# Optimization experiments

Hardware: AMD Instinct MI355X
Metric: run time of the kernel (lower is better)

## Reference

```python
import jax, jax.numpy as jnp
import numpy as np


def _soft_proto(x, P):
    d2 = (x * x).sum(-1, keepdims=True) - 2.0 * (x @ P.T) + (P * P).sum(-1)
    w = jax.nn.softmax(-d2, axis=-1)  # scores = -dist_sq, softmax over K
    return w @ P  # soft-matched prototypes


def setup_inputs() -> dict:
    key = jax.random.key(0)
    ks = jax.random.split(key, 12)
    B = 1024
    def u(k, shape, s=0.1):
        return jax.random.uniform(k, shape, minval=-s, maxval=s, dtype=jnp.float32)
    return {
        "fcn": jax.random.normal(ks[0], (B, 90, 90), jnp.float32),
        "scn": jax.random.normal(ks[1], (B, 90, 90), jnp.float32),
        # node embedding Linear(90->48), weights stored [in,out]
        "W_node": u(ks[2], (90, 48)), "b_node": jnp.zeros((48,), jnp.float32),
        "P_node": u(ks[3], (64, 48)),   # node prototypes, init uniform(-0.1,0.1)
        "W_graph": u(ks[4], (48, 32)), "b_graph": jnp.zeros((32,), jnp.float32),
        "P_graph": u(ks[5], (32, 32)),
        "Wg1": u(ks[6], (32, 32)), "bg1": jnp.zeros((32,), jnp.float32),
        "Wg2": u(ks[7], (32, 16)), "bg2": jnp.zeros((16,), jnp.float32),
        "P_cls": u(ks[8], (16, 16)),
        # classifier: final_dim = 2*90*48 + 2*32 + 2*16 = 8736
        "Wc1": u(ks[9], (8736, 256)), "bc1": jnp.zeros((256,), jnp.float32),
        "Wc2": u(ks[10], (256, 3)), "bc2": jnp.zeros((3,), jnp.float32),
    }


def reference(fcn, scn, W_node, b_node, P_node, W_graph, b_graph, P_graph,
              Wg1, bg1, Wg2, bg2, P_cls, Wc1, bc1, Wc2, bc2):
    def branch(x):
        nodes = x @ W_node + b_node                  # [B,90,48]
        nm = _soft_proto(nodes, P_node)              # [B,90,48]
        eg = nm.mean(axis=1) @ W_graph + b_graph     # [B,32]
        gp = _soft_proto(eg, P_graph)                # [B,32]
        ec = jax.nn.relu(gp @ Wg1 + bg1) @ Wg2 + bg2 # [B,16]
        cp = _soft_proto(ec, P_cls)                  # [B,16]
        return nm, gp, cp

    nmf, gpf, cpf = branch(fcn)
    nms, gps, cps = branch(scn)
    B = fcn.shape[0]
    R = jnp.concatenate(
        [nmf.reshape(B, -1), nms.reshape(B, -1), gpf, gps, cpf, cps], axis=-1)  # [B,8736]
    # dropout(0.5) is identity in eval mode
    logits = jax.nn.relu(R @ Wc1 + bc1) @ Wc2 + bc2  # [B,3]
    return logits
```

## Files before the change

kernel.cpp:

```cpp
#include <hip/hip_runtime.h>
#include <hip/hip_bf16.h>

using f16   = _Float16;
using f16x4 = __attribute__((ext_vector_type(4))) _Float16;
using f16x8 = __attribute__((ext_vector_type(8))) _Float16;
using f32x4 = __attribute__((ext_vector_type(4))) float;

__global__ __launch_bounds__(256) void prep_kernel(
    const float* __restrict__ Wn, const float* __restrict__ Pn,
    f16* __restrict__ wf, float* __restrict__ q)
{
  int i = blockIdx.x * 256 + threadIdx.x;
  if (i < 4992) {
    int n = i / 104, k = i - n * 104;
    wf[i] = (k < 90) ? (f16)Wn[k * 48 + n] : (f16)0.f;
  } else if (i < 8576) {
    int j = i - 4992; int p = j / 56, c = j - p * 56;
    wf[i] = (c < 48) ? (f16)Pn[p * 48 + c] : (f16)0.f;
  } else if (i < 12032) {
    int j = i - 8576; int r = j / 72, p = j - r * 72;
    wf[i] = (p < 64) ? (f16)Pn[p * 48 + r] : (f16)0.f;
  } else if (i < 12096) {
    int p = i - 12032;
    float s = 0.f;
    for (int j = 0; j < 48; ++j) { float v = Pn[p * 48 + j]; s = fmaf(v, v, s); }
    q[p] = s;
  }
}

__global__ __launch_bounds__(256) void wc1t_kernel(
    const float* __restrict__ Wc1, f16* __restrict__ Wc1T)
{
  __shared__ f16 sT[32 * 36];
  const int tid = threadIdx.x;
  const int kt = blockIdx.x, ct = blockIdx.y;
  const int c = tid & 31, r4 = (tid >> 5) * 4;
  #pragma unroll
  for (int i = 0; i < 4; ++i) {
    int r = r4 + i;
    sT[c * 36 + r] = (f16)Wc1[(size_t)(kt * 32 + r) * 256 + ct * 32 + c];
  }
  __syncthreads();
  #pragma unroll
  for (int i = 0; i < 4; ++i) {
    int r = r4 + i;
    Wc1T[(size_t)(ct * 32 + r) * 8736 + kt * 32 + c] = sT[r * 36 + c];
  }
}

__global__ __launch_bounds__(256, 6) void node_kernel(
    const float* __restrict__ fcn, const float* __restrict__ scn,
    const float* __restrict__ bn, const f16* __restrict__ wf,
    const float* __restrict__ qg,
    f16* __restrict__ R, float* __restrict__ nmmean)
{
  __shared__ __align__(16) f16 sW[96 * 72];
  __shared__ __align__(16) f16 sNodes[96 * 56];
  __shared__ float sQ[64];
  __shared__ float sCol[4][3][16];

  const f16* Pw   = wf + 4992;
  const f16* PnTw = wf + 8576;

  const int tid = threadIdx.x;
  const int lane = tid & 63, wv = tid >> 6;
  const int l15 = lane & 15, lg = lane >> 4;
  const int b = blockIdx.x, br = blockIdx.y;
  const float* x = (br ? scn : fcn) + (size_t)b * 8100;

  if (tid < 64) sQ[tid] = qg[tid];

  for (int mt = wv; mt < 6; mt += 4) {
    const int row = mt * 16 + l15;
    const float* xrow = x + row * 90;
    f16x8 a[3];
    #pragma unroll
    for (int kt = 0; kt < 3; ++kt) {
      const int k0 = kt * 32 + lg * 8;
      f16x8 h;
      #pragma unroll
      for (int e = 0; e < 8; ++e) h[e] = (f16)0.f;
      if (row < 90) {
        const float* src = xrow + k0;
        if (k0 < 88) {
          float2 u0 = *(const float2*)(src + 0);
          float2 u1 = *(const float2*)(src + 2);
          float2 u2 = *(const float2*)(src + 4);
          float2 u3 = *(const float2*)(src + 6);
          h[0] = (f16)u0.x; h[1] = (f16)u0.y; h[2] = (f16)u1.x; h[3] = (f16)u1.y;
          h[4] = (f16)u2.x; h[5] = (f16)u2.y; h[6] = (f16)u3.x; h[7] = (f16)u3.y;
        } else {
          float2 u0 = *(const float2*)src;
          h[0] = (f16)u0.x; h[1] = (f16)u0.y;
        }
      }
      a[kt] = h;
    }
    #pragma unroll
    for (int nt = 0; nt < 3; ++nt) {
      f32x4 acc = {0.f, 0.f, 0.f, 0.f};
      #pragma unroll
      for (int kt = 0; kt < 3; ++kt) {
        f16x8 bb = *(const f16x8*)&wf[(nt * 16 + l15) * 104 + kt * 32 + lg * 8];
        acc = __builtin_amdgcn_mfma_f32_16x16x32_f16(a[kt], bb, acc, 0, 0, 0);
      }
      const float bias = bn[nt * 16 + l15];
      #pragma unroll
      for (int r = 0; r < 4; ++r)
        sNodes[(mt * 16 + lg * 4 + r) * 56 + nt * 16 + l15] = (f16)(acc[r] + bias);
    }
  }
  __syncthreads();

  for (int mt = wv; mt < 6; mt += 4) {
    f32x4 acc[4];
    #pragma unroll
    for (int nt = 0; nt < 4; ++nt) acc[nt] = (f32x4){0.f, 0.f, 0.f, 0.f};
    const f16x8 a0 = *(const f16x8*)&sNodes[(mt * 16 + l15) * 56 + lg * 8];
    const f16x4 a1 = *(const f16x4*)&sNodes[(mt * 16 + l15) * 56 + 32 + lg * 4];
    #pragma unroll
    for (int nt = 0; nt < 4; ++nt) {
      f16x8 b0 = *(const f16x8*)&Pw[(nt * 16 + l15) * 56 + lg * 8];
      acc[nt] = __builtin_amdgcn_mfma_f32_16x16x32_f16(a0, b0, acc[nt], 0, 0, 0);
      f16x4 b1 = *(const f16x4*)&Pw[(nt * 16 + l15) * 56 + 32 + lg * 4];
      acc[nt] = __builtin_amdgcn_mfma_f32_16x16x16f16(a1, b1, acc[nt], 0, 0, 0);
    }
    float qv[4];
    #pragma unroll
    for (int nt = 0; nt < 4; ++nt) qv[nt] = sQ[nt * 16 + l15];
    #pragma unroll
    for (int r = 0; r < 4; ++r) {
      float s0 = 2.f * acc[0][r] - qv[0];
      float s1 = 2.f * acc[1][r] - qv[1];
      float s2 = 2.f * acc[2][r] - qv[2];
      float s3 = 2.f * acc[3][r] - qv[3];
      float m = fmaxf(fmaxf(s0, s1), fmaxf(s2, s3));
      m = fmaxf(m, __shfl_xor(m, 1, 64));
      m = fmaxf(m, __shfl_xor(m, 2, 64));
      m = fmaxf(m, __shfl_xor(m, 4, 64));
      m = fmaxf(m, __shfl_xor(m, 8, 64));
      float e0 = __expf(s0 - m), e1 = __expf(s1 - m);
      float e2 = __expf(s2 - m), e3 = __expf(s3 - m);
      float sum = (e0 + e1) + (e2 + e3);
      sum += __shfl_xor(sum, 1, 64);
      sum += __shfl_xor(sum, 2, 64);
      sum += __shfl_xor(sum, 4, 64);
      sum += __shfl_xor(sum, 8, 64);
      const float inv = 1.f / sum;
      const int row = mt * 16 + lg * 4 + r;
      sW[row * 72 + 0 * 16 + l15] = (f16)(e0 * inv);
      sW[row * 72 + 1 * 16 + l15] = (f16)(e1 * inv);
      sW[row * 72 + 2 * 16 + l15] = (f16)(e2 * inv);
      sW[row * 72 + 3 * 16 + l15] = (f16)(e3 * inv);
    }
  }
  __syncthreads();

  f16* Rrow = R + (size_t)b * 8736 + (size_t)br * 4320;
  float cs[3] = {0.f, 0.f, 0.f};
  for (int t = wv; t < 18; t += 4) {
    const int mt = t / 3, nt = t - 3 * mt;
    f32x4 acc = {0.f, 0.f, 0.f, 0.f};
    #pragma unroll
    for (int kt = 0; kt < 2; ++kt) {
      f16x8 a  = *(const f16x8*)&sW[(mt * 16 + l15) * 72 + kt * 32 + lg * 8];
      f16x8 bb = *(const f16x8*)&PnTw[(nt * 16 + l15) * 72 + kt * 32 + lg * 8];
      acc = __builtin_amdgcn_mfma_f32_16x16x32_f16(a, bb, acc, 0, 0, 0);
    }
    #pragma unroll
    for (int r = 0; r < 4; ++r) {
      const int row = mt * 16 + lg * 4 + r;
      if (row < 90) {
        Rrow[row * 48 + nt * 16 + l15] = (f16)acc[r];
        cs[nt] += acc[r];
      }
    }
  }
  #pragma unroll
  for (int nt = 0; nt < 3; ++nt) {
    cs[nt] += __shfl_xor(cs[nt], 16, 64);
    cs[nt] += __shfl_xor(cs[nt], 32, 64);
  }
  if (lane < 16) {
    sCol[wv][0][lane] = cs[0];
    sCol[wv][1][lane] = cs[1];
    sCol[wv][2][lane] = cs[2];
  }
  __syncthreads();
  if (tid < 48) {
    const int nt = tid >> 4, c = tid & 15;
    float s = sCol[0][nt][c] + sCol[1][nt][c] + sCol[2][nt][c] + sCol[3][nt][c];
    nmmean[((size_t)br * 1024 + b) * 48 + tid] = s * (1.f / 90.f);
  }
}

__global__ __launch_bounds__(256) void graph_kernel(
    const float* __restrict__ nmmean,
    const float* __restrict__ Wg, const float* __restrict__ bg,
    const float* __restrict__ Pg,
    const float* __restrict__ Wg1, const float* __restrict__ bg1,
    const float* __restrict__ Wg2, const float* __restrict__ bg2,
    const float* __restrict__ Pc,
    f16* __restrict__ R)
{
  __shared__ float sE[4][64];
  __shared__ float sT[4][64];
  const int tid = threadIdx.x;
  const int wid = tid >> 6, lane = tid & 63;
  const int idx = blockIdx.x * 4 + wid;
  const int br = idx >> 10, b = idx & 1023;
  const float* mrow = nmmean + (size_t)idx * 48;
  f16* Rrow = R + (size_t)b * 8736;

  if (lane < 32) {
    float e = bg[lane];
    #pragma unroll
    for (int k = 0; k < 48; ++k) e = fmaf(mrow[k], Wg[k * 32 + lane], e);
    sE[wid][lane] = e;
  }
  __syncthreads();
  if (lane < 32) {
    float s = 0.f;
    #pragma unroll
    for (int j = 0; j < 32; ++j) { float pv = Pg[lane * 32 + j]; s += pv * (2.f * sE[wid][j] - pv); }
    float m = s;
    for (int d = 16; d >= 1; d >>= 1) m = fmaxf(m, __shfl_xor(m, d, 64));
    float ex = __expf(s - m);
    float sum = ex;
    for (int d = 16; d >= 1; d >>= 1) sum += __shfl_xor(sum, d, 64);
    sT[wid][lane] = ex / sum;
  }
  __syncthreads();
  if (lane < 32) {
    float g = 0.f;
    #pragma unroll
    for (int p = 0; p < 32; ++p) g = fmaf(sT[wid][p], Pg[p * 32 + lane], g);
    Rrow[8640 + br * 32 + lane] = (f16)g;
    sE[wid][lane] = g;
  }
  __syncthreads();
  if (lane < 32) {
    float h = bg1[lane];
    #pragma unroll
    for (int k = 0; k < 32; ++k) h = fmaf(sE[wid][k], Wg1[k * 32 + lane], h);
    sT[wid][lane] = fmaxf(h, 0.f);
  }
  __syncthreads();
  if (lane < 16) {
    float c = bg2[lane];
    #pragma unroll
    for (int k = 0; k < 32; ++k) c = fmaf(sT[wid][k], Wg2[k * 16 + lane], c);
    sE[wid][lane] = c;
  }
  __syncthreads();
  if (lane < 16) {
    float s = 0.f;
    #pragma unroll
    for (int j = 0; j < 16; ++j) { float pv = Pc[lane * 16 + j]; s += pv * (2.f * sE[wid][j] - pv); }
    float m = s;
    for (int d = 8; d >= 1; d >>= 1) m = fmaxf(m, __shfl_xor(m, d, 64));
    float ex = __expf(s - m);
    float sum = ex;
    for (int d = 8; d >= 1; d >>= 1) sum += __shfl_xor(sum, d, 64);
    sT[wid][lane] = ex / sum;
  }
  __syncthreads();
  if (lane < 16) {
    float c = 0.f;
    #pragma unroll
    for (int p = 0; p < 16; ++p) c = fmaf(sT[wid][p], Pc[p * 16 + lane], c);
    Rrow[8704 + br * 16 + lane] = (f16)c;
  }
}

__global__ __launch_bounds__(256) void gemm1_kernel(
    const f16* __restrict__ R, const f16* __restrict__ Wc1T,
    float* __restrict__ part, int KS)
{
  __shared__ __align__(16) f16 sA[128 * 40];
  __shared__ __align__(16) f16 sB[64 * 40];
  const int tid = threadIdx.x;
  const int lane = tid & 63, wv = tid >> 6;
  const int l15 = lane & 15, lg = lane >> 4;
  const int wm = wv >> 1, wn = wv & 1;
  const int bm = blockIdx.x * 128, bnc = blockIdx.y * 64, z = blockIdx.z;
  const int base = 273 / KS, rem = 273 - base * KS;
  const int t0 = z * base + (z < rem ? z : rem);
  const int nt_ = base + (z < rem ? 1 : 0);
  const int kbeg = t0 * 32, kend = (t0 + nt_) * 32;

  const int ar = tid >> 1, ah = (tid & 1) * 16;
  const int bc = tid >> 2, bh = (tid & 3) * 8;

  f32x4 acc[4][2];
  #pragma unroll
  for (int mt = 0; mt < 4; ++mt)
    #pragma unroll
    for (int nt = 0; nt < 2; ++nt) acc[mt][nt] = (f32x4){0.f, 0.f, 0.f, 0.f};

  f16x8 v0 = *(const f16x8*)&R[(size_t)(bm + ar) * 8736 + kbeg + ah];
  f16x8 v1 = *(const f16x8*)&R[(size_t)(bm + ar) * 8736 + kbeg + ah + 8];
  f16x8 w0 = *(const f16x8*)&Wc1T[(size_t)(bnc + bc) * 8736 + kbeg + bh];

  for (int kk = kbeg; kk < kend; kk += 32) {
    *(f16x8*)&sA[ar * 40 + ah] = v0;
    *(f16x8*)&sA[ar * 40 + ah + 8] = v1;
    *(f16x8*)&sB[bc * 40 + bh] = w0;
    __syncthreads();
    if (kk + 32 < kend) {
      v0 = *(const f16x8*)&R[(size_t)(bm + ar) * 8736 + kk + 32 + ah];
      v1 = *(const f16x8*)&R[(size_t)(bm + ar) * 8736 + kk + 32 + ah + 8];
      w0 = *(const f16x8*)&Wc1T[(size_t)(bnc + bc) * 8736 + kk + 32 + bh];
    }
    #pragma unroll
    for (int mt = 0; mt < 4; ++mt) {
      f16x8 a = *(const f16x8*)&sA[(wm * 64 + mt * 16 + l15) * 40 + lg * 8];
      #pragma unroll
      for (int nt = 0; nt < 2; ++nt) {
        f16x8 bb = *(const f16x8*)&sB[(wn * 32 + nt * 16 + l15) * 40 + lg * 8];
        acc[mt][nt] = __builtin_amdgcn_mfma_f32_16x16x32_f16(a, bb, acc[mt][nt], 0, 0, 0);
      }
    }
    __syncthreads();
  }
  float* pz = part + (size_t)z * 262144;
  #pragma unroll
  for (int mt = 0; mt < 4; ++mt)
    #pragma unroll
    for (int nt = 0; nt < 2; ++nt)
      #pragma unroll
      for (int r = 0; r < 4; ++r)
        pz[(size_t)(bm + wm * 64 + mt * 16 + lg * 4 + r) * 256 +
           bnc + wn * 32 + nt * 16 + l15] = acc[mt][nt][r];
}

__global__ __launch_bounds__(256) void head_kernel(
    const float* __restrict__ part, const float* __restrict__ bc1,
    const float* __restrict__ Wc2, const float* __restrict__ bc2,
    float* __restrict__ out, int KS)
{
  __shared__ float red[3][4];
  const int b = blockIdx.x, t = threadIdx.x;
  float s0 = 0.f, s1 = 0.f, s2 = 0.f, s3 = 0.f;
  int z = 0;
  for (; z + 4 <= KS; z += 4) {
    s0 += part[(size_t)(z + 0) * 262144 + (size_t)b * 256 + t];
    s1 += part[(size_t)(z + 1) * 262144 + (size_t)b * 256 + t];
    s2 += part[(size_t)(z + 2) * 262144 + (size_t)b * 256 + t];
    s3 += part[(size_t)(z + 3) * 262144 + (size_t)b * 256 + t];
  }
  for (; z < KS; ++z) s0 += part[(size_t)z * 262144 + (size_t)b * 256 + t];
  float acc = bc1[t] + ((s0 + s1) + (s2 + s3));
  float h = fmaxf(acc, 0.f);
  float p0 = h * Wc2[t * 3 + 0];
  float p1 = h * Wc2[t * 3 + 1];
  float p2 = h * Wc2[t * 3 + 2];
  for (int d = 32; d >= 1; d >>= 1) {
    p0 += __shfl_xor(p0, d, 64);
    p1 += __shfl_xor(p1, d, 64);
    p2 += __shfl_xor(p2, d, 64);
  }
  const int wid = t >> 6, lane = t & 63;
  if (lane == 0) { red[0][wid] = p0; red[1][wid] = p1; red[2][wid] = p2; }
  __syncthreads();
  if (t < 3) {
    out[(size_t)b * 3 + t] = red[t][0] + red[t][1] + red[t][2] + red[t][3] + bc2[t];
  }
}

extern "C" void kernel_launch(void* const* d_in, const int* in_sizes, int n_in,
                              void* d_out, int out_size, void* d_ws, size_t ws_size,
                              hipStream_t stream) {
  const float* fcn     = (const float*)d_in[0];
  const float* scn     = (const float*)d_in[1];
  const float* W_node  = (const float*)d_in[2];
  const float* b_node  = (const float*)d_in[3];
  const float* P_node  = (const float*)d_in[4];
  const float* W_graph = (const float*)d_in[5];
  const float* b_graph = (const float*)d_in[6];
  const float* P_graph = (const float*)d_in[7];
  const float* Wg1     = (const float*)d_in[8];
  const float* bg1     = (const float*)d_in[9];
  const float* Wg2     = (const float*)d_in[10];
  const float* bg2     = (const float*)d_in[11];
  const float* P_cls   = (const float*)d_in[12];
  const float* Wc1     = (const float*)d_in[13];
  const float* bc1     = (const float*)d_in[14];
  const float* Wc2     = (const float*)d_in[15];
  const float* bc2     = (const float*)d_in[16];
  float* out = (float*)d_out;

  char* ws = (char*)d_ws;
  f16*   R16    = (f16*)ws;
  f16*   Wc1T   = (f16*)(ws + 17891328);
  f16*   wf     = (f16*)(ws + 22364160);
  float* qbuf   = (float*)(ws + 22388224);
  float* nmmean = (float*)(ws + 22388480);
  float* part   = (float*)(ws + 22781696);

  size_t avail = ws_size > 22781696u ? ws_size - 22781696u : 0;
  int KS = (int)(avail / 1048576u);
  if (KS > 16) KS = 16;
  if (KS < 1) KS = 1;

  prep_kernel<<<48, 256, 0, stream>>>(W_node, P_node, wf, qbuf);
  wc1t_kernel<<<dim3(273, 8), 256, 0, stream>>>(Wc1, Wc1T);
  node_kernel<<<dim3(1024, 2), 256, 0, stream>>>(fcn, scn, b_node, wf, qbuf,
                                                 R16, nmmean);
  graph_kernel<<<512, 256, 0, stream>>>(nmmean, W_graph, b_graph, P_graph,
                                        Wg1, bg1, Wg2, bg2, P_cls, R16);
  gemm1_kernel<<<dim3(8, 4, KS), 256, 0, stream>>>(R16, Wc1T, part, KS);
  head_kernel<<<1024, 256, 0, stream>>>(part, bc1, Wc2, bc2, out, KS);
}
```

Baseline: 70.15 us.

## Give each wave one 16-row tile in node kernel and drop block barriers

The node kernel now launches 384 threads so each of six waves owns one 16-row tile through all three stages: node embedding, prototype softmax and soft-match output. Intermediates sit in a per-wave shared scratch and are guarded only by lgkmcnt waits, which removes two block-wide __syncthreads and the imbalance of 4 waves covering 6 tiles. It also cuts shared memory per block and reads q straight from global. The risk is lower occupancy from the larger block size and the removed launch_bounds min-blocks hint, which may raise register use.

```diff
diff --git a/kernel.cpp b/kernel.cpp
--- a/kernel.cpp
+++ b/kernel.cpp
@@ -48,16 +48,15 @@
   }
 }
 
-__global__ __launch_bounds__(256, 6) void node_kernel(
+__global__ __launch_bounds__(384) void node_kernel(
     const float* __restrict__ fcn, const float* __restrict__ scn,
     const float* __restrict__ bn, const f16* __restrict__ wf,
     const float* __restrict__ qg,
     f16* __restrict__ R, float* __restrict__ nmmean)
 {
-  __shared__ __align__(16) f16 sW[96 * 72];
-  __shared__ __align__(16) f16 sNodes[96 * 56];
+  __shared__ __align__(16) f16 sS[6][1152];
   __shared__ float sQ[64];
-  __shared__ float sCol[4][3][16];
+  __shared__ float sCol[6][3][16];
 
   const f16* Pw   = wf + 4992;
   const f16* PnTw = wf + 8576;
@@ -67,111 +66,110 @@
   const int l15 = lane & 15, lg = lane >> 4;
   const int b = blockIdx.x, br = blockIdx.y;
   const float* x = (br ? scn : fcn) + (size_t)b * 8100;
+  f16* scr = sS[wv];
 
   if (tid < 64) sQ[tid] = qg[tid];
 
-  for (int mt = wv; mt < 6; mt += 4) {
-    const int row = mt * 16 + l15;
-    const float* xrow = x + row * 90;
-    f16x8 a[3];
+  const int row = wv * 16 + l15;
+  const float* xrow = x + row * 90;
+  f16x8 a[3];
+  #pragma unroll
+  for (int kt = 0; kt < 3; ++kt) {
+    const int k0 = kt * 32 + lg * 8;
+    f16x8 h;
+    #pragma unroll
+    for (int e = 0; e < 8; ++e) h[e] = (f16)0.f;
+    if (row < 90) {
+      const float* src = xrow + k0;
+      if (k0 < 88) {
+        float2 u0 = *(const float2*)(src + 0);
+        float2 u1 = *(const float2*)(src + 2);
+        float2 u2 = *(const float2*)(src + 4);
+        float2 u3 = *(const float2*)(src + 6);
+        h[0] = (f16)u0.x; h[1] = (f16)u0.y; h[2] = (f16)u1.x; h[3] = (f16)u1.y;
+        h[4] = (f16)u2.x; h[5] = (f16)u2.y; h[6] = (f16)u3.x; h[7] = (f16)u3.y;
+      } else {
+        float2 u0 = *(const float2*)src;
+        h[0] = (f16)u0.x; h[1] = (f16)u0.y;
+      }
+    }
+    a[kt] = h;
+  }
+  #pragma unroll
+  for (int nt = 0; nt < 3; ++nt) {
+    f32x4 acc = {0.f, 0.f, 0.f, 0.f};
     #pragma unroll
     for (int kt = 0; kt < 3; ++kt) {
-      const int k0 = kt * 32 + lg * 8;
-      f16x8 h;
-      #pragma unroll
-      for (int e = 0; e < 8; ++e) h[e] = (f16)0.f;
-      if (row < 90) {
-        const float* src = xrow + k0;
-        if (k0 < 88) {
-          float2 u0 = *(const float2*)(src + 0);
-          float2 u1 = *(const float2*)(src + 2);
-          float2 u2 = *(const float2*)(src + 4);
-          float2 u3 = *(const float2*)(src + 6);
-          h[0] = (f16)u0.x; h[1] = (f16)u0.y; h[2] = (f16)u1.x; h[3] = (f16)u1.y;
-          h[4] = (f16)u2.x; h[5] = (f16)u2.y; h[6] = (f16)u3.x; h[7] = (f16)u3.y;
-        } else {
-          float2 u0 = *(const float2*)src;
-          h[0] = (f16)u0.x; h[1] = (f16)u0.y;
-        }
-      }
-      a[kt] = h;
+      f16x8 bb = *(const f16x8*)&wf[(nt * 16 + l15) * 104 + kt * 32 + lg * 8];
+      acc = __builtin_amdgcn_mfma_f32_16x16x32_f16(a[kt], bb, acc, 0, 0, 0);
     }
-    #pragma unroll
-    for (int nt = 0; nt < 3; ++nt) {
-      f32x4 acc = {0.f, 0.f, 0.f, 0.f};
-      #pragma unroll
-      for (int kt = 0; kt < 3; ++kt) {
-        f16x8 bb = *(const f16x8*)&wf[(nt * 16 + l15) * 104 + kt * 32 + lg * 8];
-        acc = __builtin_amdgcn_mfma_f32_16x16x32_f16(a[kt], bb, acc, 0, 0, 0);
-      }
-      const float bias = bn[nt * 16 + l15];
-      #pragma unroll
-      for (int r = 0; r < 4; ++r)
-        sNodes[(mt * 16 + lg * 4 + r) * 56 + nt * 16 + l15] = (f16)(acc[r] + bias);
-    }
-  }
-  __syncthreads();
-
-  for (int mt = wv; mt < 6; mt += 4) {
-    f32x4 acc[4];
-    #pragma unroll
-    for (int nt = 0; nt < 4; ++nt) acc[nt] = (f32x4){0.f, 0.f, 0.f, 0.f};
-    const f16x8 a0 = *(const f16x8*)&sNodes[(mt * 16 + l15) * 56 + lg * 8];
-    const f16x4 a1 = *(const f16x4*)&sNodes[(mt * 16 + l15) * 56 + 32 + lg * 4];
-    #pragma unroll
-    for (int nt = 0; nt < 4; ++nt) {
-      f16x8 b0 = *(const f16x8*)&Pw[(nt * 16 + l15) * 56 + lg * 8];
-      acc[nt] = __builtin_amdgcn_mfma_f32_16x16x32_f16(a0, b0, acc[nt], 0, 0, 0);
-      f16x4 b1 = *(const f16x4*)&Pw[(nt * 16 + l15) * 56 + 32 + lg * 4];
-      acc[nt] = __builtin_amdgcn_mfma_f32_16x16x16f16(a1, b1, acc[nt], 0, 0, 0);
-    }
-    float qv[4];
-    #pragma unroll
-    for (int nt = 0; nt < 4; ++nt) qv[nt] = sQ[nt * 16 + l15];
+    const float bias = bn[nt * 16 + l15];
+    #pragma unroll
+    for (int r = 0; r < 4; ++r)
+      scr[(lg * 4 + r) * 56 + nt * 16 + l15] = (f16)(acc[r] + bias);
+  }
+  asm volatile("s_waitcnt lgkmcnt(0)" ::: "memory");
+  __builtin_amdgcn_sched_barrier(0);
+
+  const f16x8 a0 = *(const f16x8*)&scr[l15 * 56 + lg * 8];
+  const f16x4 a1 = *(const f16x4*)&scr[l15 * 56 + 32 + lg * 4];
+  f32x4 acc2[4];
+  #pragma unroll
+  for (int nt = 0; nt < 4; ++nt) acc2[nt] = (f32x4){0.f, 0.f, 0.f, 0.f};
+  #pragma unroll
+  for (int nt = 0; nt < 4; ++nt) {
+    f16x8 b0 = *(const f16x8*)&Pw[(nt * 16 + l15) * 56 + lg * 8];
+    acc2[nt] = __builtin_amdgcn_mfma_f32_16x16x32_f16(a0, b0, acc2[nt], 0, 0, 0);
+    f16x4 b1 = *(const f16x4*)&Pw[(nt * 16 + l15) * 56 + 32 + lg * 4];
+    acc2[nt] = __builtin_amdgcn_mfma_f32_16x16x16f16(a1, b1, acc2[nt], 0, 0, 0);
+  }
+  float qv[4];
+  #pragma unroll
+  for (int nt = 0; nt < 4; ++nt) qv[nt] = qg[nt * 16 + l15];
+  #pragma unroll
+  for (int r = 0; r < 4; ++r) {
+    float s0 = 2.f * acc2[0][r] - qv[0];
+    float s1 = 2.f * acc2[1][r] - qv[1];
+    float s2 = 2.f * acc2[2][r] - qv[2];
+    float s3 = 2.f * acc2[3][r] - qv[3];
+    float m = fmaxf(fmaxf(s0, s1), fmaxf(s2, s3));
+    m = fmaxf(m, __shfl_xor(m, 1, 64));
+    m = fmaxf(m, __shfl_xor(m, 2, 64));
+    m = fmaxf(m, __shfl_xor(m, 4, 64));
+    m = fmaxf(m, __shfl_xor(m, 8, 64));
+    float e0 = __expf(s0 - m), e1 = __expf(s1 - m);
+    float e2 = __expf(s2 - m), e3 = __expf(s3 - m);
+    float sum = (e0 + e1) + (e2 + e3);
+    sum += __shfl_xor(sum, 1, 64);
+    sum += __shfl_xor(sum, 2, 64);
+    sum += __shfl_xor(sum, 4, 64);
+    sum += __shfl_xor(sum, 8, 64);
+    const float inv = 1.f / sum;
+    const int lr = lg * 4 + r;
+    scr[lr * 72 + 0 * 16 + l15] = (f16)(e0 * inv);
+    scr[lr * 72 + 1 * 16 + l15] = (f16)(e1 * inv);
+    scr[lr * 72 + 2 * 16 + l15] = (f16)(e2 * inv);
+    scr[lr * 72 + 3 * 16 + l15] = (f16)(e3 * inv);
+  }
+  asm volatile("s_waitcnt lgkmcnt(0)" ::: "memory");
+  __builtin_amdgcn_sched_barrier(0);
+
+  f16* Rrow = R + (size_t)b * 8736 + (size_t)br * 4320;
+  const f16x8 wa0 = *(const f16x8*)&scr[l15 * 72 + lg * 8];
+  const f16x8 wa1 = *(const f16x8*)&scr[l15 * 72 + 32 + lg * 8];
+  float cs[3] = {0.f, 0.f, 0.f};
+  #pragma unroll
+  for (int nt = 0; nt < 3; ++nt) {
+    f32x4 acc = {0.f, 0.f, 0.f, 0.f};
+    f16x8 b0 = *(const f16x8*)&PnTw[(nt * 16 + l15) * 72 + lg * 8];
+    acc = __builtin_amdgcn_mfma_f32_16x16x32_f16(wa0, b0, acc, 0, 0, 0);
+    f16x8 b1 = *(const f16x8*)&PnTw[(nt * 16 + l15) * 72 + 32 + lg * 8];
+    acc = __builtin_amdgcn_mfma_f32_16x16x32_f16(wa1, b1, acc, 0, 0, 0);
     #pragma unroll
     for (int r = 0; r < 4; ++r) {
-      float s0 = 2.f * acc[0][r] - qv[0];
-      float s1 = 2.f * acc[1][r] - qv[1];
-      float s2 = 2.f * acc[2][r] - qv[2];
-      float s3 = 2.f * acc[3][r] - qv[3];
-      float m = fmaxf(fmaxf(s0, s1), fmaxf(s2, s3));
-      m = fmaxf(m, __shfl_xor(m, 1, 64));
-      m = fmaxf(m, __shfl_xor(m, 2, 64));
-      m = fmaxf(m, __shfl_xor(m, 4, 64));
-      m = fmaxf(m, __shfl_xor(m, 8, 64));
-      float e0 = __expf(s0 - m), e1 = __expf(s1 - m);
-      float e2 = __expf(s2 - m), e3 = __expf(s3 - m);
-      float sum = (e0 + e1) + (e2 + e3);
-      sum += __shfl_xor(sum, 1, 64);
-      sum += __shfl_xor(sum, 2, 64);
-      sum += __shfl_xor(sum, 4, 64);
-      sum += __shfl_xor(sum, 8, 64);
-      const float inv = 1.f / sum;
-      const int row = mt * 16 + lg * 4 + r;
-      sW[row * 72 + 0 * 16 + l15] = (f16)(e0 * inv);
-      sW[row * 72 + 1 * 16 + l15] = (f16)(e1 * inv);
-      sW[row * 72 + 2 * 16 + l15] = (f16)(e2 * inv);
-      sW[row * 72 + 3 * 16 + l15] = (f16)(e3 * inv);
-    }
-  }
-  __syncthreads();
-
-  f16* Rrow = R + (size_t)b * 8736 + (size_t)br * 4320;
-  float cs[3] = {0.f, 0.f, 0.f};
-  for (int t = wv; t < 18; t += 4) {
-    const int mt = t / 3, nt = t - 3 * mt;
-    f32x4 acc = {0.f, 0.f, 0.f, 0.f};
-    #pragma unroll
-    for (int kt = 0; kt < 2; ++kt) {
-      f16x8 a  = *(const f16x8*)&sW[(mt * 16 + l15) * 72 + kt * 32 + lg * 8];
-      f16x8 bb = *(const f16x8*)&PnTw[(nt * 16 + l15) * 72 + kt * 32 + lg * 8];
-      acc = __builtin_amdgcn_mfma_f32_16x16x32_f16(a, bb, acc, 0, 0, 0);
-    }
-    #pragma unroll
-    for (int r = 0; r < 4; ++r) {
-      const int row = mt * 16 + lg * 4 + r;
-      if (row < 90) {
-        Rrow[row * 48 + nt * 16 + l15] = (f16)acc[r];
+      const int grow = wv * 16 + lg * 4 + r;
+      if (grow < 90) {
+        Rrow[grow * 48 + nt * 16 + l15] = (f16)acc[r];
         cs[nt] += acc[r];
       }
     }
@@ -189,7 +187,9 @@
   __syncthreads();
   if (tid < 48) {
     const int nt = tid >> 4, c = tid & 15;
-    float s = sCol[0][nt][c] + sCol[1][nt][c] + sCol[2][nt][c] + sCol[3][nt][c];
+    float s = 0.f;
+    #pragma unroll
+    for (int w = 0; w < 6; ++w) s += sCol[w][nt][c];
     nmmean[((size_t)br * 1024 + b) * 48 + tid] = s * (1.f / 90.f);
   }
 }
@@ -405,7 +405,7 @@
 
   prep_kernel<<<48, 256, 0, stream>>>(W_node, P_node, wf, qbuf);
   wc1t_kernel<<<dim3(273, 8), 256, 0, stream>>>(Wc1, Wc1T);
-  node_kernel<<<dim3(1024, 2), 256, 0, stream>>>(fcn, scn, b_node, wf, qbuf,
+  node_kernel<<<dim3(1024, 2), 384, 0, stream>>>(fcn, scn, b_node, wf, qbuf,
                                                  R16, nmmean);
   graph_kernel<<<512, 256, 0, stream>>>(nmmean, W_graph, b_graph, P_graph,
                                         Wg1, bg1, Wg2, bg2, P_cls, R16);
```

Result: no change. 71.44 us (+1.8%).
